# Kernel tuning notes

Measured on AMD Instinct MI355X. Metric: run time of the kernel, lower is better.

## Reference

```python
import jax, jax.numpy as jnp
import numpy as np

B, L, E, D1, D2 = 256, 128, 64, 512, 512


def setup_inputs() -> dict:
    key = jax.random.key(0)
    k1, k2, k3, kw = jax.random.split(key, 4)
    tensor1 = jax.random.normal(k1, (B, L, D1), dtype=jnp.float32)
    tensor2 = jax.random.normal(k2, (B, L, D2), dtype=jnp.float32)
    parameters_index = jax.random.randint(k3, (B,), 0, E, dtype=jnp.int32)
    # xavier_uniform with relu gain: gain*sqrt(6/(fan_in+fan_out)),
    # torch fan for [E,D1,D2]: fan_in = D1*D2, fan_out = E*D2
    gain = float(np.sqrt(2.0))
    bound = gain * float(np.sqrt(6.0 / (D1 * D2 + E * D2)))
    weights = jax.random.uniform(kw, (E, D1, D2), minval=-bound, maxval=bound, dtype=jnp.float32)
    return {"tensor1": tensor1, "tensor2": tensor2, "parameters_index": parameters_index, "weights": weights}


def reference(tensor1, tensor2, parameters_index, weights):
    # gather per-batch weight matrix [B, D1, D2], then bilinear form x1^T W x2
    w = weights[parameters_index]  # [B, D1, D2]
    # equals: sum over i,j of tensor1[b,l,i] * w[b,i,j] * tensor2[b,l,j] -> [B, L]
    return jnp.einsum('bli,bij,blj->bl', tensor1, w, tensor2)
```

## Files before the change

kernel.cpp:

```cpp
#include <hip/hip_runtime.h>
#include <stdint.h>

#define NB 256
#define NL 128
#define ND1 512
#define ND2 512

#define BI 128
#define BK 64
#define NKT (ND2 / BK)
#define LDST 72

typedef float float4_t __attribute__((ext_vector_type(4)));
typedef __bf16 bf16x8_t __attribute__((ext_vector_type(8)));
typedef unsigned short ushort4_t __attribute__((ext_vector_type(4)));
typedef unsigned short ushort8_t __attribute__((ext_vector_type(8)));

__device__ __forceinline__ unsigned short f2bf(float f) {
    unsigned int u = __float_as_uint(f);
    u += 0x7FFFu + ((u >> 16) & 1u);
    return (unsigned short)(u >> 16);
}

__global__ __launch_bounds__(256, 4) void pdot_kernel(
    const float* __restrict__ t1, const float* __restrict__ t2,
    const int* __restrict__ pidx, const float* __restrict__ wgt,
    float* __restrict__ out)
{
    __shared__ unsigned short sA[NL * LDST];
    __shared__ unsigned short sB[BI * LDST];

    const int g  = blockIdx.x;
    const int b  = g & (NB - 1);
    const int it = g >> 8;
    const int i0 = it * BI;

    const int t  = threadIdx.x;
    const int wv = t >> 6;
    const int ln = t & 63;
    const int nh = ln & 15;
    const int qd = ln >> 4;

    const int e = pidx[b];
    const float* aPtr  = t2  + (size_t)b * (NL * ND2);
    const float* bPtr  = wgt + (size_t)e * (ND1 * ND2) + (size_t)i0 * ND2;
    const float* t1p   = t1  + (size_t)b * (NL * ND1) + i0;

    float4_t acc[2][8];
    #pragma unroll
    for (int i = 0; i < 2; ++i)
        #pragma unroll
        for (int j = 0; j < 8; ++j) {
            float4_t z = {0.f, 0.f, 0.f, 0.f};
            acc[i][j] = z;
        }

    const int s_row = t >> 4;
    const int s_kq  = (t & 15) * 4;

    for (int kt = 0; kt < NKT; ++kt) {
        const int k0 = kt * BK;

        #pragma unroll
        for (int p = 0; p < 8; ++p) {
            const int row = p * 16 + s_row;
            float4_t va = *(const float4_t*)(aPtr + (size_t)row * ND2 + (k0 + s_kq));
            float4_t vb = *(const float4_t*)(bPtr + (size_t)row * ND2 + (k0 + s_kq));
            ushort4_t ua, ub;
            ua.x = f2bf(va.x); ua.y = f2bf(va.y); ua.z = f2bf(va.z); ua.w = f2bf(va.w);
            ub.x = f2bf(vb.x); ub.y = f2bf(vb.y); ub.z = f2bf(vb.z); ub.w = f2bf(vb.w);
            *(ushort4_t*)(&sA[row * LDST + s_kq]) = ua;
            *(ushort4_t*)(&sB[row * LDST + s_kq]) = ub;
        }

        __syncthreads();

        #pragma unroll
        for (int ks = 0; ks < 2; ++ks) {
            const int kf = ks * 32 + qd * 8;
            bf16x8_t af[2];
            bf16x8_t bfr[8];
            #pragma unroll
            for (int ms = 0; ms < 2; ++ms) {
                const int row = wv * 32 + ms * 16 + nh;
                af[ms] = __builtin_bit_cast(bf16x8_t, *(ushort8_t*)(&sA[row * LDST + kf]));
            }
            #pragma unroll
            for (int ns = 0; ns < 8; ++ns) {
                const int nr = ns * 16 + nh;
                bfr[ns] = __builtin_bit_cast(bf16x8_t, *(ushort8_t*)(&sB[nr * LDST + kf]));
            }
            #pragma unroll
            for (int ms = 0; ms < 2; ++ms)
                #pragma unroll
                for (int ns = 0; ns < 8; ++ns)
                    acc[ms][ns] = __builtin_amdgcn_mfma_f32_16x16x32_bf16(af[ms], bfr[ns], acc[ms][ns], 0, 0, 0);
        }

        __syncthreads();
    }

    #pragma unroll
    for (int ms = 0; ms < 2; ++ms) {
        #pragma unroll
        for (int r = 0; r < 4; ++r) {
            const int row = wv * 32 + ms * 16 + qd * 4 + r;
            float ps = 0.f;
            #pragma unroll
            for (int ns = 0; ns < 8; ++ns) {
                const float tv = t1p[(size_t)row * ND1 + ns * 16 + nh];
                ps += acc[ms][ns][r] * tv;
            }
            ps += __shfl_xor(ps, 1);
            ps += __shfl_xor(ps, 2);
            ps += __shfl_xor(ps, 4);
            ps += __shfl_xor(ps, 8);
            if (nh == 0) atomicAdd(&out[b * NL + row], ps);
        }
    }
}

extern "C" void kernel_launch(void* const* d_in, const int* in_sizes, int n_in,
                              void* d_out, int out_size, void* d_ws, size_t ws_size,
                              hipStream_t stream)
{
    const float* t1  = (const float*)d_in[0];
    const float* t2  = (const float*)d_in[1];
    const int* pidx  = (const int*)d_in[2];
    const float* wgt = (const float*)d_in[3];
    float* out = (float*)d_out;

    hipMemsetAsync(out, 0, (size_t)out_size * sizeof(float), stream);
    pdot_kernel<<<dim3(NB * (ND1 / BI)), dim3(256), 0, stream>>>(t1, t2, pidx, wgt, out);
}
```

Before: 242.6 us.

## Double-buffer LDS tiles with register prefetch and halve the K tile

The K loop now uses two LDS buffers and prefetches the next global tile into registers while MFMAs run on the current buffer, so only one barrier is needed per iteration. BK shrinks from 64 to 32 and LDS padding from 72 to 40, so the two buffers fit in roughly the same shared memory. The aim is to hide global load latency behind compute. In exchange the kernel runs twice as many iterations, each with less work, and holds more registers for the prefetched data, which under launch_bounds(256,4) may cause spills.

```diff
diff --git a/kernel.cpp b/kernel.cpp
--- a/kernel.cpp
+++ b/kernel.cpp
@@ -7,9 +7,9 @@
 #define ND2 512
 
 #define BI 128
-#define BK 64
+#define BK 32
 #define NKT (ND2 / BK)
-#define LDST 72
+#define LDST 40
 
 typedef float float4_t __attribute__((ext_vector_type(4)));
 typedef __bf16 bf16x8_t __attribute__((ext_vector_type(8)));
@@ -27,8 +27,8 @@
     const int* __restrict__ pidx, const float* __restrict__ wgt,
     float* __restrict__ out)
 {
-    __shared__ unsigned short sA[NL * LDST];
-    __shared__ unsigned short sB[BI * LDST];
+    __shared__ unsigned short sA[2][NL * LDST];
+    __shared__ unsigned short sB[2][BI * LDST];
 
     const int g  = blockIdx.x;
     const int b  = g & (NB - 1);
@@ -42,9 +42,9 @@
     const int qd = ln >> 4;
 
     const int e = pidx[b];
-    const float* aPtr  = t2  + (size_t)b * (NL * ND2);
-    const float* bPtr  = wgt + (size_t)e * (ND1 * ND2) + (size_t)i0 * ND2;
-    const float* t1p   = t1  + (size_t)b * (NL * ND1) + i0;
+    const float* aPtr = t2  + (size_t)b * (NL * ND2);
+    const float* bPtr = wgt + (size_t)e * (ND1 * ND2) + (size_t)i0 * ND2;
+    const float* t1p  = t1  + (size_t)b * (NL * ND1) + i0;
 
     float4_t acc[2][8];
     #pragma unroll
@@ -55,48 +55,76 @@
             acc[i][j] = z;
         }
 
-    const int s_row = t >> 4;
-    const int s_kq  = (t & 15) * 4;
+    const int rq = t >> 3;
+    const int cq = (t & 7) * 4;
 
-    for (int kt = 0; kt < NKT; ++kt) {
-        const int k0 = kt * BK;
+    const float* aRow = aPtr + (size_t)rq * ND2 + cq;
+    const float* bRow = bPtr + (size_t)rq * ND2 + cq;
 
+    float4_t ra[4], rb[4];
+
+    const int kf = qd * 8;
+
+    #pragma unroll
+    for (int q = 0; q < 4; ++q) {
+        ra[q] = *(const float4_t*)(aRow + (size_t)q * 32 * ND2);
+        rb[q] = *(const float4_t*)(bRow + (size_t)q * 32 * ND2);
+    }
+    #pragma unroll
+    for (int q = 0; q < 4; ++q) {
+        ushort4_t ua, ub;
+        ua.x = f2bf(ra[q].x); ua.y = f2bf(ra[q].y); ua.z = f2bf(ra[q].z); ua.w = f2bf(ra[q].w);
+        ub.x = f2bf(rb[q].x); ub.y = f2bf(rb[q].y); ub.z = f2bf(rb[q].z); ub.w = f2bf(rb[q].w);
+        *(ushort4_t*)(&sA[0][(rq + q * 32) * LDST + cq]) = ua;
+        *(ushort4_t*)(&sB[0][(rq + q * 32) * LDST + cq]) = ub;
+    }
+    #pragma unroll
+    for (int q = 0; q < 4; ++q) {
+        ra[q] = *(const float4_t*)(aRow + (size_t)q * 32 * ND2 + BK);
+        rb[q] = *(const float4_t*)(bRow + (size_t)q * 32 * ND2 + BK);
+    }
+    __syncthreads();
+
+    for (int i = 0; i < NKT; ++i) {
+        const int cur = i & 1;
+
+        bf16x8_t af[2];
+        bf16x8_t bfr[8];
         #pragma unroll
-        for (int p = 0; p < 8; ++p) {
-            const int row = p * 16 + s_row;
-            float4_t va = *(const float4_t*)(aPtr + (size_t)row * ND2 + (k0 + s_kq));
-            float4_t vb = *(const float4_t*)(bPtr + (size_t)row * ND2 + (k0 + s_kq));
-            ushort4_t ua, ub;
-            ua.x = f2bf(va.x); ua.y = f2bf(va.y); ua.z = f2bf(va.z); ua.w = f2bf(va.w);
-            ub.x = f2bf(vb.x); ub.y = f2bf(vb.y); ub.z = f2bf(vb.z); ub.w = f2bf(vb.w);
-            *(ushort4_t*)(&sA[row * LDST + s_kq]) = ua;
-            *(ushort4_t*)(&sB[row * LDST + s_kq]) = ub;
+        for (int ms = 0; ms < 2; ++ms) {
+            const int row = wv * 32 + ms * 16 + nh;
+            af[ms] = __builtin_bit_cast(bf16x8_t, *(ushort8_t*)(&sA[cur][row * LDST + kf]));
         }
+        #pragma unroll
+        for (int ns = 0; ns < 8; ++ns) {
+            const int nr = ns * 16 + nh;
+            bfr[ns] = __builtin_bit_cast(bf16x8_t, *(ushort8_t*)(&sB[cur][nr * LDST + kf]));
+        }
+        #pragma unroll
+        for (int ms = 0; ms < 2; ++ms)
+            #pragma unroll
+            for (int ns = 0; ns < 8; ++ns)
+                acc[ms][ns] = __builtin_amdgcn_mfma_f32_16x16x32_bf16(af[ms], bfr[ns], acc[ms][ns], 0, 0, 0);
 
-        __syncthreads();
-
-        #pragma unroll
-        for (int ks = 0; ks < 2; ++ks) {
-            const int kf = ks * 32 + qd * 8;
-            bf16x8_t af[2];
-            bf16x8_t bfr[8];
+        if (i < NKT - 1) {
+            const int nxt = cur ^ 1;
             #pragma unroll
-            for (int ms = 0; ms < 2; ++ms) {
-                const int row = wv * 32 + ms * 16 + nh;
-                af[ms] = __builtin_bit_cast(bf16x8_t, *(ushort8_t*)(&sA[row * LDST + kf]));
+            for (int q = 0; q < 4; ++q) {
+                ushort4_t ua, ub;
+                ua.x = f2bf(ra[q].x); ua.y = f2bf(ra[q].y); ua.z = f2bf(ra[q].z); ua.w = f2bf(ra[q].w);
+                ub.x = f2bf(rb[q].x); ub.y = f2bf(rb[q].y); ub.z = f2bf(rb[q].z); ub.w = f2bf(rb[q].w);
+                *(ushort4_t*)(&sA[nxt][(rq + q * 32) * LDST + cq]) = ua;
+                *(ushort4_t*)(&sB[nxt][(rq + q * 32) * LDST + cq]) = ub;
             }
-            #pragma unroll
-            for (int ns = 0; ns < 8; ++ns) {
-                const int nr = ns * 16 + nh;
-                bfr[ns] = __builtin_bit_cast(bf16x8_t, *(ushort8_t*)(&sB[nr * LDST + kf]));
+            if (i < NKT - 2) {
+                const size_t ko = (size_t)(i + 2) * BK;
+                #pragma unroll
+                for (int q = 0; q < 4; ++q) {
+                    ra[q] = *(const float4_t*)(aRow + (size_t)q * 32 * ND2 + ko);
+                    rb[q] = *(const float4_t*)(bRow + (size_t)q * 32 * ND2 + ko);
+                }
             }
-            #pragma unroll
-            for (int ms = 0; ms < 2; ++ms)
-                #pragma unroll
-                for (int ns = 0; ns < 8; ++ns)
-                    acc[ms][ns] = __builtin_amdgcn_mfma_f32_16x16x32_bf16(af[ms], bfr[ns], acc[ms][ns], 0, 0, 0);
         }
-
         __syncthreads();
     }
 
```

Result: slower. 277.6 us (+14.4%).

## Stage whole weight slice in swizzled LDS and stream t2 fragments from global

Applied to the files above, without the earlier changes.

Each block now converts a 64-row slice of the selected weight matrix to bf16 once and keeps it in a 64KB XOR-swizzled shared-memory buffer. The t2 operand is no longer staged through shared memory. Each lane loads its MFMA A-fragment directly from global memory, with a one-step register prefetch, so the per-k-tile double __syncthreads loop goes away. Blocks grow to 512 threads, the i-tile shrinks from 128 to 64 rows, and the grid doubles. The trade-off is that t2 is re-read by twice as many blocks, the global loads are less coalesced, and the large shared-memory footprint limits occupancy.

```diff
diff --git a/kernel.cpp b/kernel.cpp
--- a/kernel.cpp
+++ b/kernel.cpp
@@ -6,14 +6,11 @@
 #define ND1 512
 #define ND2 512
 
-#define BI 128
-#define BK 64
-#define NKT (ND2 / BK)
-#define LDST 72
+#define BI 64
+#define NKT 16
 
 typedef float float4_t __attribute__((ext_vector_type(4)));
 typedef __bf16 bf16x8_t __attribute__((ext_vector_type(8)));
-typedef unsigned short ushort4_t __attribute__((ext_vector_type(4)));
 typedef unsigned short ushort8_t __attribute__((ext_vector_type(8)));
 
 __device__ __forceinline__ unsigned short f2bf(float f) {
@@ -22,13 +19,12 @@
     return (unsigned short)(u >> 16);
 }
 
-__global__ __launch_bounds__(256, 4) void pdot_kernel(
+__global__ __launch_bounds__(512, 4) void pdot_kernel(
     const float* __restrict__ t1, const float* __restrict__ t2,
     const int* __restrict__ pidx, const float* __restrict__ wgt,
     float* __restrict__ out)
 {
-    __shared__ unsigned short sA[NL * LDST];
-    __shared__ unsigned short sB[BI * LDST];
+    __shared__ unsigned short sW[BI * ND2];
 
     const int g  = blockIdx.x;
     const int b  = g & (NB - 1);
@@ -42,81 +38,73 @@
     const int qd = ln >> 4;
 
     const int e = pidx[b];
-    const float* aPtr  = t2  + (size_t)b * (NL * ND2);
-    const float* bPtr  = wgt + (size_t)e * (ND1 * ND2) + (size_t)i0 * ND2;
-    const float* t1p   = t1  + (size_t)b * (NL * ND1) + i0;
+    const float* wp = wgt + (size_t)e * (ND1 * ND2) + (size_t)i0 * ND2;
 
-    float4_t acc[2][8];
+    {
+        const int r  = t >> 3;
+        const int c8 = t & 7;
+        const int sw = r & 7;
+        const float* src = wp + (size_t)r * ND2;
+        unsigned short* dst = &sW[r * ND2];
+        #pragma unroll
+        for (int q = 0; q < 8; ++q) {
+            const int c = c8 + 8 * q;
+            float4_t lo = *(const float4_t*)(src + c * 8);
+            float4_t hi = *(const float4_t*)(src + c * 8 + 4);
+            ushort8_t u;
+            u[0] = f2bf(lo.x); u[1] = f2bf(lo.y); u[2] = f2bf(lo.z); u[3] = f2bf(lo.w);
+            u[4] = f2bf(hi.x); u[5] = f2bf(hi.y); u[6] = f2bf(hi.z); u[7] = f2bf(hi.w);
+            *(ushort8_t*)(dst + ((c ^ sw) * 8)) = u;
+        }
+    }
+    __syncthreads();
+
+    const float* aRow = t2 + (size_t)b * (NL * ND2) + (size_t)(wv * 16 + nh) * ND2;
+    const int swz = nh & 7;
+    const unsigned short* wBase = &sW[nh * ND2];
+
+    float4_t acc[4];
     #pragma unroll
-    for (int i = 0; i < 2; ++i)
+    for (int ns = 0; ns < 4; ++ns) { float4_t z = {0.f,0.f,0.f,0.f}; acc[ns] = z; }
+
+    float4_t a_lo = *(const float4_t*)(aRow + qd * 8);
+    float4_t a_hi = *(const float4_t*)(aRow + qd * 8 + 4);
+
+    #pragma unroll
+    for (int kt = 0; kt < NKT; ++kt) {
+        float4_t n_lo, n_hi;
+        if (kt < NKT - 1) {
+            n_lo = *(const float4_t*)(aRow + (kt + 1) * 32 + qd * 8);
+            n_hi = *(const float4_t*)(aRow + (kt + 1) * 32 + qd * 8 + 4);
+        }
+        ushort8_t ua;
+        ua[0] = f2bf(a_lo.x); ua[1] = f2bf(a_lo.y); ua[2] = f2bf(a_lo.z); ua[3] = f2bf(a_lo.w);
+        ua[4] = f2bf(a_hi.x); ua[5] = f2bf(a_hi.y); ua[6] = f2bf(a_hi.z); ua[7] = f2bf(a_hi.w);
+        bf16x8_t af = __builtin_bit_cast(bf16x8_t, ua);
+
+        const int co = ((kt * 4 + qd) ^ swz) * 8;
         #pragma unroll
-        for (int j = 0; j < 8; ++j) {
-            float4_t z = {0.f, 0.f, 0.f, 0.f};
-            acc[i][j] = z;
+        for (int ns = 0; ns < 4; ++ns) {
+            bf16x8_t bfr = __builtin_bit_cast(bf16x8_t,
+                *(const ushort8_t*)(wBase + ns * 16 * ND2 + co));
+            acc[ns] = __builtin_amdgcn_mfma_f32_16x16x32_bf16(af, bfr, acc[ns], 0, 0, 0);
         }
-
-    const int s_row = t >> 4;
-    const int s_kq  = (t & 15) * 4;
-
-    for (int kt = 0; kt < NKT; ++kt) {
-        const int k0 = kt * BK;
-
-        #pragma unroll
-        for (int p = 0; p < 8; ++p) {
-            const int row = p * 16 + s_row;
-            float4_t va = *(const float4_t*)(aPtr + (size_t)row * ND2 + (k0 + s_kq));
-            float4_t vb = *(const float4_t*)(bPtr + (size_t)row * ND2 + (k0 + s_kq));
-            ushort4_t ua, ub;
-            ua.x = f2bf(va.x); ua.y = f2bf(va.y); ua.z = f2bf(va.z); ua.w = f2bf(va.w);
-            ub.x = f2bf(vb.x); ub.y = f2bf(vb.y); ub.z = f2bf(vb.z); ub.w = f2bf(vb.w);
-            *(ushort4_t*)(&sA[row * LDST + s_kq]) = ua;
-            *(ushort4_t*)(&sB[row * LDST + s_kq]) = ub;
-        }
-
-        __syncthreads();
-
-        #pragma unroll
-        for (int ks = 0; ks < 2; ++ks) {
-            const int kf = ks * 32 + qd * 8;
-            bf16x8_t af[2];
-            bf16x8_t bfr[8];
-            #pragma unroll
-            for (int ms = 0; ms < 2; ++ms) {
-                const int row = wv * 32 + ms * 16 + nh;
-                af[ms] = __builtin_bit_cast(bf16x8_t, *(ushort8_t*)(&sA[row * LDST + kf]));
-            }
-            #pragma unroll
-            for (int ns = 0; ns < 8; ++ns) {
-                const int nr = ns * 16 + nh;
-                bfr[ns] = __builtin_bit_cast(bf16x8_t, *(ushort8_t*)(&sB[nr * LDST + kf]));
-            }
-            #pragma unroll
-            for (int ms = 0; ms < 2; ++ms)
-                #pragma unroll
-                for (int ns = 0; ns < 8; ++ns)
-                    acc[ms][ns] = __builtin_amdgcn_mfma_f32_16x16x32_bf16(af[ms], bfr[ns], acc[ms][ns], 0, 0, 0);
-        }
-
-        __syncthreads();
+        a_lo = n_lo; a_hi = n_hi;
     }
 
+    const float* t1p = t1 + (size_t)b * (NL * ND1) + i0;
     #pragma unroll
-    for (int ms = 0; ms < 2; ++ms) {
+    for (int r = 0; r < 4; ++r) {
+        const int row = wv * 16 + qd * 4 + r;
+        float ps = 0.f;
         #pragma unroll
-        for (int r = 0; r < 4; ++r) {
-            const int row = wv * 32 + ms * 16 + qd * 4 + r;
-            float ps = 0.f;
-            #pragma unroll
-            for (int ns = 0; ns < 8; ++ns) {
-                const float tv = t1p[(size_t)row * ND1 + ns * 16 + nh];
-                ps += acc[ms][ns][r] * tv;
-            }
-            ps += __shfl_xor(ps, 1);
-            ps += __shfl_xor(ps, 2);
-            ps += __shfl_xor(ps, 4);
-            ps += __shfl_xor(ps, 8);
-            if (nh == 0) atomicAdd(&out[b * NL + row], ps);
-        }
+        for (int ns = 0; ns < 4; ++ns)
+            ps += acc[ns][r] * t1p[(size_t)row * ND1 + ns * 16 + nh];
+        ps += __shfl_xor(ps, 1);
+        ps += __shfl_xor(ps, 2);
+        ps += __shfl_xor(ps, 4);
+        ps += __shfl_xor(ps, 8);
+        if (nh == 0) atomicAdd(&out[b * NL + row], ps);
     }
 }
 
@@ -131,5 +119,5 @@
     float* out = (float*)d_out;
 
     hipMemsetAsync(out, 0, (size_t)out_size * sizeof(float), stream);
-    pdot_kernel<<<dim3(NB * (ND1 / BI)), dim3(256), 0, stream>>>(t1, t2, pidx, wgt, out);
+    pdot_kernel<<<dim3(NB * (ND1 / BI)), dim3(512), 0, stream>>>(t1, t2, pidx, wgt, out);
 }
```

Measured after the change: 245.9 us. About the same (+1.4%).
